# Kernel tuning notes

Measured on AMD Instinct MI355X. Metric: run time of the kernel, lower is better.

Reference implementation:

```python
import jax, jax.numpy as jnp
import numpy as np

COL = 14
NJ = 23
SIGMA = 1.0
RADIUS = int(4.0 * SIGMA + 0.5)  # scipy gaussian_filter default truncate=4.0


def _gauss_matrix(col=COL, sigma=SIGMA, radius=RADIUS):
    """col x col matrix M such that (M @ img @ M.T) == scipy gaussian_filter(img, sigma)
    with scipy's default 'reflect' boundary (== numpy 'symmetric')."""
    xs = np.arange(-radius, radius + 1)
    w = np.exp(-0.5 * (xs / sigma) ** 2)
    w = (w / w.sum()).astype(np.float32)
    M = np.zeros((col, col), np.float32)
    for out in range(col):
        for k in range(-radius, radius + 1):
            i = (out + k) % (2 * col)
            if i >= col:
                i = 2 * col - 1 - i
            M[out, i] += w[k + radius]
    return M

_M = jnp.asarray(_gauss_matrix())


def setup_inputs() -> dict:
    key = jax.random.key(0)
    k0, k1, k2, k3 = jax.random.split(key, 4)
    B = 4096
    o = jax.random.normal(k0, (B, 3 * NJ, COL, COL), dtype=jnp.float32)
    h = jax.random.uniform(k1, (B, NJ, COL, COL), dtype=jnp.float32)
    t = jax.random.uniform(k2, (B, NJ, 3), dtype=jnp.float32)
    v = jax.random.randint(k3, (B, NJ, 2), 0, 2, dtype=jnp.int32)
    return {"o": o, "h": h, "t": t, "v": v}


def reference(o, h, t, v):
    B = h.shape[0]
    scale = 1.0 / COL

    # per-joint argmax over the heatmap -> integer (y, x) coords
    idx = jnp.argmax(h.reshape(B, NJ, COL * COL), axis=-1)  # [B, Nj]
    y = idx // COL
    x = idx % COL

    bi = jnp.arange(B)[:, None]
    ji = jnp.arange(NJ)[None, :]
    px = o[bi, ji, y, x] + x.astype(h.dtype) * scale
    py = o[bi, ji + NJ, y, x] + y.astype(h.dtype) * scale
    pz = o[bi, ji + 2 * NJ, y, x]
    pred = jnp.stack([px, py, pz], axis=-1)  # [B, Nj, 3]

    # target heatmaps: delta at (yi, xi), gaussian-filtered, min-max normalized
    ti = t * COL
    xi = jnp.trunc(ti[..., 0]).astype(jnp.int32)  # int() truncation as in torch code
    yi = jnp.trunc(ti[..., 1]).astype(jnp.int32)
    in_range = (xi >= 0) & (xi <= COL - 1) & (yi >= 0) & (yi <= COL - 1)
    mask = (v[..., 0] == 1) & in_range  # [B, Nj]

    xc = jnp.clip(xi, 0, COL - 1)
    yc = jnp.clip(yi, 0, COL - 1)
    # gaussian_filter of a one-hot delta is the outer product of two filter columns
    gy = _M.T[yc]  # [B, Nj, COL], gy[..., r] = M[r, yc]
    gx = _M.T[xc]  # [B, Nj, COL]
    tt_map = gy[..., :, None] * gx[..., None, :]  # [B, Nj, COL, COL]
    mn = tt_map.min(axis=(-2, -1), keepdims=True)
    mx = tt_map.max(axis=(-2, -1), keepdims=True)
    tt = (tt_map - mn) / (mx - mn)
    tt = tt * mask[..., None, None].astype(h.dtype)

    d1 = jnp.sum((h - tt) ** 2) / NJ
    d2 = jnp.sum((pred - t) ** 2) / NJ
    return d1 + d2
```

## Files before the change

### kernel.cpp

```cpp
#include <hip/hip_runtime.h>
#include <math.h>

#define COL 14
#define NJ 23
#define BATCH 4096
#define NJOINT (BATCH * NJ)
#define RADIUS 4
#define THREADS 256
#define BLOCKS 1472
#define WAVES_TOTAL (BLOCKS * (THREADS / 64))

__global__ __launch_bounds__(THREADS) void msq3d_kernel(
    const float* __restrict__ o,
    const float* __restrict__ h,
    const float* __restrict__ t,
    const int*   __restrict__ v,
    float* __restrict__ out)
{
    __shared__ float sM[COL * COL];
    __shared__ float sColMin[COL], sColMax[COL];
    __shared__ float sWaveSum[THREADS / 64];

    const int tid = threadIdx.x;

    if (tid < COL * COL) {
        double wd[2 * RADIUS + 1];
        double wsum = 0.0;
        #pragma unroll
        for (int k = 0; k <= 2 * RADIUS; ++k) {
            double xx = (double)(k - RADIUS);
            wd[k] = exp(-0.5 * xx * xx);
            wsum += wd[k];
        }
        const int outr = tid / COL, ic = tid % COL;
        float acc = 0.0f;
        #pragma unroll
        for (int k = -RADIUS; k <= RADIUS; ++k) {
            int ii = (outr + k) % (2 * COL);
            if (ii < 0) ii += 2 * COL;
            if (ii >= COL) ii = 2 * COL - 1 - ii;
            if (ii == ic) acc += (float)(wd[k + RADIUS] / wsum);
        }
        sM[outr * COL + ic] = acc;
    }
    __syncthreads();
    if (tid < COL) {
        float mn = sM[tid], mx = mn;
        for (int r = 1; r < COL; ++r) {
            float x = sM[r * COL + tid];
            mn = fminf(mn, x);
            mx = fmaxf(mx, x);
        }
        sColMin[tid] = mn;
        sColMax[tid] = mx;
    }
    __syncthreads();

    const int lane = tid & 63;
    const int wave_in_blk = tid >> 6;
    const int gwave = blockIdx.x * (THREADS / 64) + wave_in_blk;
    const float scale = 1.0f / (float)COL;

    const bool act = (lane < 49);
    const int q0 = lane * 4;
    int rk[4], ck[4];
    #pragma unroll
    for (int k = 0; k < 4; ++k) {
        int q = q0 + k;
        if (q > COL * COL - 1) q = COL * COL - 1;
        rk[k] = q / COL;
        ck[k] = q - rk[k] * COL;
    }

    float accD = 0.0f;

    int joint = gwave;
    float4 hv4 = make_float4(0.f, 0.f, 0.f, 0.f);
    {
        const float4* hb4 = (const float4*)(h + (size_t)joint * (COL * COL));
        if (act) hv4 = hb4[lane];
    }
    float t0 = t[joint * 3 + 0];
    float t1 = t[joint * 3 + 1];
    float t2 = t[joint * 3 + 2];
    int   v0 = v[joint * 2 + 0];

    for (;;) {
        const int jn = joint + WAVES_TOTAL;
        const bool more = (jn < NJOINT);
        float4 nh4 = make_float4(0.f, 0.f, 0.f, 0.f);
        float nt0 = 0.f, nt1 = 0.f, nt2 = 0.f;
        int   nv0 = 0;
        if (more) {
            const float4* nb4 = (const float4*)(h + (size_t)jn * (COL * COL));
            if (act) nh4 = nb4[lane];
            nt0 = t[jn * 3 + 0];
            nt1 = t[jn * 3 + 1];
            nt2 = t[jn * 3 + 2];
            nv0 = v[jn * 2 + 0];
        }

        const int b = joint / NJ;
        const int j = joint - b * NJ;

        const int xi = (int)truncf(t0 * (float)COL);
        const int yi = (int)truncf(t1 * (float)COL);
        const bool in_range = (xi >= 0) && (xi <= COL - 1) && (yi >= 0) && (yi <= COL - 1);
        const bool mask = (v0 == 1) && in_range;
        const int xc = min(max(xi, 0), COL - 1);
        const int yc = min(max(yi, 0), COL - 1);

        const float hv[4] = {hv4.x, hv4.y, hv4.z, hv4.w};

        float lv = -INFINITY;
        int   lq = 0;
        if (act) {
            #pragma unroll
            for (int k = 0; k < 4; ++k) {
                if (hv[k] > lv) { lv = hv[k]; lq = q0 + k; }
            }
        }

        if (mask) {
            const float mn  = sColMin[yc] * sColMin[xc];
            const float mx  = sColMax[yc] * sColMax[xc];
            const float inv = 1.0f / (mx - mn);
            if (act) {
                #pragma unroll
                for (int k = 0; k < 4; ++k) {
                    float ttv = (sM[rk[k] * COL + yc] * sM[ck[k] * COL + xc] - mn) * inv;
                    float d = hv[k] - ttv;
                    accD += d * d;
                }
            }
        } else if (act) {
            #pragma unroll
            for (int k = 0; k < 4; ++k)
                accD += hv[k] * hv[k];
        }

        float wmax = lv;
        #pragma unroll
        for (int off = 1; off < 64; off <<= 1)
            wmax = fmaxf(wmax, __shfl_xor(wmax, off, 64));
        unsigned long long mb = __ballot(act && (lv == wmax));
        const int src = (int)(__ffsll((long long)mb) - 1);
        const int besti = __shfl(lq, src, 64);

        const int by = besti / COL;
        const int bx = besti - by * COL;
        if (lane < 3) {
            const size_t ob = (((size_t)b * (3 * NJ) + j + lane * NJ) * COL + by) * COL + bx;
            const float ov = o[ob];
            const float addv = (lane == 0) ? (float)bx * scale
                             : (lane == 1) ? (float)by * scale : 0.0f;
            const float tc = (lane == 0) ? t0 : (lane == 1) ? t1 : t2;
            const float d = (ov + addv) - tc;
            accD += d * d;
        }

        if (!more) break;
        joint = jn;
        hv4 = nh4;
        t0 = nt0; t1 = nt1; t2 = nt2; v0 = nv0;
    }

    #pragma unroll
    for (int off = 32; off > 0; off >>= 1)
        accD += __shfl_down(accD, off, 64);
    if (lane == 0) sWaveSum[wave_in_blk] = accD;
    __syncthreads();
    if (tid == 0) {
        float s = 0.0f;
        #pragma unroll
        for (int w = 0; w < THREADS / 64; ++w) s += sWaveSum[w];
        atomicAdd(out, s * (1.0f / (float)NJ));
    }
}

extern "C" void kernel_launch(void* const* d_in, const int* in_sizes, int n_in,
                              void* d_out, int out_size, void* d_ws, size_t ws_size,
                              hipStream_t stream) {
    const float* o = (const float*)d_in[0];
    const float* h = (const float*)d_in[1];
    const float* t = (const float*)d_in[2];
    const int*   v = (const int*)d_in[3];
    float* out = (float*)d_out;

    hipMemsetAsync(d_out, 0, sizeof(float), stream);
    msq3d_kernel<<<BLOCKS, THREADS, 0, stream>>>(o, h, t, v, out);
}
```

Measured before the change: 320.8 us.

## Defer gathered o loads, use DPP wave max, fixed-trip loop with pointer strides

```diff
diff --git a/kernel.cpp b/kernel.cpp
--- a/kernel.cpp
+++ b/kernel.cpp
@@ -9,8 +9,26 @@
 #define THREADS 256
 #define BLOCKS 1472
 #define WAVES_TOTAL (BLOCKS * (THREADS / 64))
-
-__global__ __launch_bounds__(THREADS) void msq3d_kernel(
+#define JPW (NJOINT / WAVES_TOTAL)
+
+__device__ __forceinline__ float wave_max_f32(float x) {
+    int xi;
+    xi = __builtin_amdgcn_update_dpp(__float_as_int(x), __float_as_int(x), 0xB1, 0xF, 0xF, true);
+    x = fmaxf(x, __int_as_float(xi));
+    xi = __builtin_amdgcn_update_dpp(__float_as_int(x), __float_as_int(x), 0x4E, 0xF, 0xF, true);
+    x = fmaxf(x, __int_as_float(xi));
+    xi = __builtin_amdgcn_update_dpp(__float_as_int(x), __float_as_int(x), 0x141, 0xF, 0xF, true);
+    x = fmaxf(x, __int_as_float(xi));
+    xi = __builtin_amdgcn_update_dpp(__float_as_int(x), __float_as_int(x), 0x140, 0xF, 0xF, true);
+    x = fmaxf(x, __int_as_float(xi));
+    xi = __builtin_amdgcn_ds_swizzle(__float_as_int(x), 0x401F);
+    x = fmaxf(x, __int_as_float(xi));
+    const float a = __int_as_float(__builtin_amdgcn_readlane(__float_as_int(x), 0));
+    const float b = __int_as_float(__builtin_amdgcn_readlane(__float_as_int(x), 32));
+    return fmaxf(a, b);
+}
+
+__global__ __launch_bounds__(THREADS, 6) void msq3d_kernel(
     const float* __restrict__ o,
     const float* __restrict__ h,
     const float* __restrict__ t,
@@ -72,41 +90,45 @@
         ck[k] = q - rk[k] * COL;
     }
 
+    const int b0 = gwave / NJ;
+    const int j0 = gwave - b0 * NJ;
+
+    const float4* hp = (const float4*)(h + (size_t)gwave * (COL * COL)) + lane;
+    const float*  tp = t + (size_t)gwave * 3;
+    const int*    vp = v + (size_t)gwave * 2;
+    const size_t  HSTRIDE = (size_t)WAVES_TOTAL * (COL * COL) / 4;
+    const size_t  OSTRIDE = (size_t)256 * (3 * NJ) * (COL * COL);
+    size_t obase = ((size_t)b0 * (3 * NJ) + j0 + (size_t)(lane < 3 ? lane : 0) * NJ) * (COL * COL);
+
     float accD = 0.0f;
 
-    int joint = gwave;
     float4 hv4 = make_float4(0.f, 0.f, 0.f, 0.f);
-    {
-        const float4* hb4 = (const float4*)(h + (size_t)joint * (COL * COL));
-        if (act) hv4 = hb4[lane];
-    }
-    float t0 = t[joint * 3 + 0];
-    float t1 = t[joint * 3 + 1];
-    float t2 = t[joint * 3 + 2];
-    int   v0 = v[joint * 2 + 0];
-
-    for (;;) {
-        const int jn = joint + WAVES_TOTAL;
-        const bool more = (jn < NJOINT);
+    if (act) hv4 = *hp;
+    hp += HSTRIDE;
+    float t0 = tp[0], t1 = tp[1], t2 = tp[2];
+    int   v0 = vp[0];
+    tp += (size_t)WAVES_TOTAL * 3;
+    vp += (size_t)WAVES_TOTAL * 2;
+
+    float pov = 0.f, pc = 0.f;
+
+    #pragma unroll 1
+    for (int i = 0; i < JPW; ++i) {
         float4 nh4 = make_float4(0.f, 0.f, 0.f, 0.f);
         float nt0 = 0.f, nt1 = 0.f, nt2 = 0.f;
         int   nv0 = 0;
-        if (more) {
-            const float4* nb4 = (const float4*)(h + (size_t)jn * (COL * COL));
-            if (act) nh4 = nb4[lane];
-            nt0 = t[jn * 3 + 0];
-            nt1 = t[jn * 3 + 1];
-            nt2 = t[jn * 3 + 2];
-            nv0 = v[jn * 2 + 0];
-        }
-
-        const int b = joint / NJ;
-        const int j = joint - b * NJ;
+        if (i + 1 < JPW) {
+            if (act) nh4 = *hp;
+            nt0 = tp[0]; nt1 = tp[1]; nt2 = tp[2];
+            nv0 = vp[0];
+        }
+        hp += HSTRIDE;
+        tp += (size_t)WAVES_TOTAL * 3;
+        vp += (size_t)WAVES_TOTAL * 2;
 
         const int xi = (int)truncf(t0 * (float)COL);
         const int yi = (int)truncf(t1 * (float)COL);
-        const bool in_range = (xi >= 0) && (xi <= COL - 1) && (yi >= 0) && (yi <= COL - 1);
-        const bool mask = (v0 == 1) && in_range;
+        const bool mask = (v0 == 1) && (xi >= 0) && (xi <= COL - 1) && (yi >= 0) && (yi <= COL - 1);
         const int xc = min(max(xi, 0), COL - 1);
         const int yc = min(max(yi, 0), COL - 1);
 
@@ -139,30 +161,33 @@
                 accD += hv[k] * hv[k];
         }
 
-        float wmax = lv;
-        #pragma unroll
-        for (int off = 1; off < 64; off <<= 1)
-            wmax = fmaxf(wmax, __shfl_xor(wmax, off, 64));
+        const float wmax = wave_max_f32(lv);
         unsigned long long mb = __ballot(act && (lv == wmax));
         const int src = (int)(__ffsll((long long)mb) - 1);
-        const int besti = __shfl(lq, src, 64);
+        const int besti = __builtin_amdgcn_readlane(lq, src);
+
+        if (lane < 3) {
+            const float d = pov + pc;
+            accD += d * d;
+        }
 
         const int by = besti / COL;
         const int bx = besti - by * COL;
         if (lane < 3) {
-            const size_t ob = (((size_t)b * (3 * NJ) + j + lane * NJ) * COL + by) * COL + bx;
-            const float ov = o[ob];
-            const float addv = (lane == 0) ? (float)bx * scale
-                             : (lane == 1) ? (float)by * scale : 0.0f;
-            const float tc = (lane == 0) ? t0 : (lane == 1) ? t1 : t2;
-            const float d = (ov + addv) - tc;
-            accD += d * d;
-        }
-
-        if (!more) break;
-        joint = jn;
+            pov = o[obase + (size_t)(by * COL + bx)];
+            pc = (lane == 0) ? ((float)bx * scale - t0)
+               : (lane == 1) ? ((float)by * scale - t1)
+               : (-t2);
+        }
+        obase += OSTRIDE;
+
         hv4 = nh4;
         t0 = nt0; t1 = nt1; t2 = nt2; v0 = nv0;
+    }
+
+    if (lane < 3) {
+        const float d = pov + pc;
+        accD += d * d;
     }
 
     #pragma unroll
```

Result: no change. 320.4 us (-0.1%).
